# Performance work log

Measured on AMD Instinct MI355X. Metric: run time of the kernel, lower is better.

The kernel has to match this reference:

```python
import jax, jax.numpy as jnp
import numpy as np

N_HEAD = 16
HEAD_DIM = 64

def setup_inputs() -> dict:
    key = jax.random.key(0)
    k1, k2, k3 = jax.random.split(key, 3)
    B, S, D = 4, 2048, 1024
    x = jax.random.normal(k1, (B, S, D), dtype=jnp.float32)
    mask = jnp.tril(jnp.ones((S, S), dtype=bool))[None, None]  # (1,1,S,S) causal
    w_attn = jax.random.normal(k2, (D, 3 * D), dtype=jnp.float32) * (1.0 / np.sqrt(D))
    b_attn = jnp.zeros((3 * D,), dtype=jnp.float32)
    w_proj = jax.random.normal(k3, (D, D), dtype=jnp.float32) * (1.0 / np.sqrt(D))
    b_proj = jnp.zeros((D,), dtype=jnp.float32)
    return {"x": x, "mask": mask, "w_attn": w_attn, "b_attn": b_attn,
            "w_proj": w_proj, "b_proj": b_proj}

def reference(x, mask, w_attn, b_attn, w_proj, b_proj):
    B, S, D = x.shape
    H, hd = N_HEAD, HEAD_DIM
    qkv = x @ w_attn + b_attn                      # (B,S,3D)
    q, k, v = jnp.split(qkv, 3, axis=-1)
    q = q.reshape(B, S, H, hd).transpose(0, 2, 1, 3)  # (B,H,S,hd)
    k = k.reshape(B, S, H, hd).transpose(0, 2, 1, 3)
    v = v.reshape(B, S, H, hd).transpose(0, 2, 1, 3)
    scores = jnp.einsum('bhqd,bhkd->bhqk', q, k) / jnp.sqrt(jnp.float32(hd))
    scores = jnp.where(mask, scores, jnp.float32(-1e10))
    weights = jax.nn.softmax(scores, axis=-1)      # dropout is identity (deterministic=True)
    attn = jnp.einsum('bhqk,bhkd->bhqd', weights, v)
    attn = attn.transpose(0, 2, 1, 3).reshape(B, S, D)
    return attn @ w_proj + b_proj
```

## Files before the change

kernel.cpp:

```cpp
#include <hip/hip_runtime.h>
#include <hip/hip_bf16.h>
#include <stdint.h>


typedef uint16_t u16;
typedef __bf16 bf16x8 __attribute__((ext_vector_type(8)));
typedef __bf16 bf16x4 __attribute__((ext_vector_type(4)));
typedef short s16x4 __attribute__((ext_vector_type(4)));
typedef float f32x4 __attribute__((ext_vector_type(4)));

#define S_LEN 2048
#define DMODEL 1024
#define NHEAD 16
#define HDIM 64
#define MTOT 8192
#define NQKV 3072

__device__ __forceinline__ u16 f2bf(float f) {
    union { float f; uint32_t u; } v; v.f = f;
    uint32_t u = v.u;
    return (u16)((u + 0x7fffu + ((u >> 16) & 1u)) >> 16);
}

__device__ __forceinline__ s16x4 bits4(bf16x4 v) {
    union { bf16x4 b; s16x4 s; } u; u.b = v; return u.s;
}

__device__ __forceinline__ f32x4 mfma16(bf16x4 a, bf16x4 b, f32x4 c) {
    return __builtin_amdgcn_mfma_f32_16x16x16bf16_1k(bits4(a), bits4(b), c, 0, 0, 0);
}

__device__ __forceinline__ void async_load16(const void* g, void* l) {
    __builtin_amdgcn_global_load_lds(
        (__attribute__((address_space(1))) void*)g,
        (__attribute__((address_space(3))) void*)l,
        16, 0, 0);
}

__global__ void convert_x_kernel(const float4* __restrict__ in, ushort4* __restrict__ out, int n4) {
    int i = blockIdx.x * 256 + threadIdx.x;
    if (i < n4) {
        float4 f = in[i];
        ushort4 o;
        o.x = f2bf(f.x); o.y = f2bf(f.y); o.z = f2bf(f.z); o.w = f2bf(f.w);
        out[i] = o;
    }
}

__global__ void transpose_bf16_kernel(const float* __restrict__ in, u16* __restrict__ out, int R, int C) {
    __shared__ float tile[64][65];
    int r0 = blockIdx.y * 64, c0 = blockIdx.x * 64;
    #pragma unroll
    for (int i = 0; i < 16; ++i) {
        int idx = threadIdx.x + i * 256;
        int r = idx >> 6, c = idx & 63;
        tile[r][c] = in[(size_t)(r0 + r) * C + c0 + c];
    }
    __syncthreads();
    #pragma unroll
    for (int i = 0; i < 16; ++i) {
        int idx = threadIdx.x + i * 256;
        int c = idx >> 6, r = idx & 63;
        out[(size_t)(c0 + c) * R + r0 + r] = f2bf(tile[r][c]);
    }
}

__global__ void transpose_v_kernel(const u16* __restrict__ qkv, u16* __restrict__ vt) {
    __shared__ u16 tile[64 * 66];
    const int tid = threadIdx.x;
    const int stile = blockIdx.x, bh = blockIdx.y;
    const int b = bh >> 4, h = bh & 15;
    const u16* src = qkv + ((size_t)b * S_LEN + stile * 64) * NQKV + 2 * DMODEL + h * HDIM;
    #pragma unroll
    for (int it = 0; it < 2; ++it) {
        int item = it * 256 + tid;
        int s = item >> 3, d0 = (item & 7) * 8;
        bf16x8 v = *(const bf16x8*)(src + (size_t)s * NQKV + d0);
        const u16* vu = (const u16*)&v;
        #pragma unroll
        for (int j = 0; j < 8; ++j) tile[(d0 + j) * 66 + s] = vu[j];
    }
    __syncthreads();
    #pragma unroll
    for (int it = 0; it < 2; ++it) {
        int item = it * 256 + tid;
        int d = item >> 3, s0 = (item & 7) * 8;
        union { u16 u[8]; uint4 v; } pk;
        #pragma unroll
        for (int j = 0; j < 8; ++j) pk.u[j] = tile[d * 66 + s0 + j];
        *(uint4*)(vt + ((size_t)bh * 64 + d) * S_LEN + stile * 64 + s0) = pk.v;
    }
}

template<bool OUT_BF16>
__global__ __launch_bounds__(512, 2) void gemm256sq(
    const u16* __restrict__ A, const u16* __restrict__ Bt,
    const float* __restrict__ bias, void* __restrict__ C,
    int M, int N, int K)
{
    __shared__ __attribute__((aligned(16))) u16 sm[65536];
    u16* const As = sm;
    u16* const Bs = sm + 32768;

    const int tid = threadIdx.x;
    const int wave = tid >> 6, lane = tid & 63;
    const int l15 = lane & 15, q4 = lane >> 4;
    const int wm = wave >> 2, wn = wave & 3;

    const int bid = (int)blockIdx.x;
    const int xcd = bid & 7;
    const int lx  = bid >> 3;
    const int MB  = M >> 8;
    const int PM  = MB >> 3;
    const int nb  = lx / PM;
    const int mb  = xcd * PM + (lx - nb * PM);
    const int m0 = mb << 8, n0 = nb << 8;

    const u16* Ag = A + (size_t)m0 * K;
    const u16* Bg = Bt + (size_t)n0 * K;

    const int srow = tid >> 3;
    const size_t goff0 = (size_t)srow * K + (size_t)(((tid & 7) ^ (srow & 7)) * 8);
    const size_t goff1 = goff0 + (size_t)64 * K;
    const int ldso = tid * 8;

    const int ck0 = (q4 ^ (l15 & 7)) * 8;
    const int ck1 = ((4 + q4) ^ (l15 & 7)) * 8;
    const int rb0 = (wn * 64 + l15) * 64;

    f32x4 acc[8][4] = {};
    const int T = K >> 6;

#define STAGE_A(t_, h_) do { \
    const u16* g_ = Ag + (size_t)(h_) * 128 * K + (size_t)(t_) * 64; \
    u16* d_ = As + (((t_) & 1) * 2 + (h_)) * 8192; \
    async_load16(g_ + goff0, d_ + ldso); \
    async_load16(g_ + goff1, d_ + ldso + 4096); \
} while (0)

#define STAGE_B(t_, h_) do { \
    const u16* g_ = Bg + (size_t)(h_) * 128 * K + (size_t)(t_) * 64; \
    u16* d_ = Bs + ((t_) & 1) * 16384 + (h_) * 8192; \
    async_load16(g_ + goff0, d_ + ldso); \
    async_load16(g_ + goff1, d_ + ldso + 4096); \
} while (0)

#define LOAD_AF(P_) do { \
    af[0][0] = *(const bf16x8*)(Ah + ((2 * (P_)) * 16 + l15) * 64 + ck0); \
    af[0][1] = *(const bf16x8*)(Ah + ((2 * (P_)) * 16 + l15) * 64 + ck1); \
    af[1][0] = *(const bf16x8*)(Ah + ((2 * (P_) + 1) * 16 + l15) * 64 + ck0); \
    af[1][1] = *(const bf16x8*)(Ah + ((2 * (P_) + 1) * 16 + l15) * 64 + ck1); \
} while (0)

#define PHASE_MFMA(P_) do { \
    asm volatile("s_barrier" ::: "memory"); \
    __builtin_amdgcn_s_setprio(1); \
    _Pragma("unroll") \
    for (int i_ = 0; i_ < 2; ++i_) \
        _Pragma("unroll") \
        for (int nf_ = 0; nf_ < 4; ++nf_) \
            _Pragma("unroll") \
            for (int kk_ = 0; kk_ < 2; ++kk_) \
                acc[2 * (P_) + i_][nf_] = __builtin_amdgcn_mfma_f32_16x16x32_bf16( \
                    af[i_][kk_], bfr[nf_][kk_], acc[2 * (P_) + i_][nf_], 0, 0, 0); \
    __builtin_amdgcn_s_setprio(0); \
} while (0)

    STAGE_A(0, 0); STAGE_A(0, 1); STAGE_B(0, 0); STAGE_B(0, 1);
    if (T > 1) {
        STAGE_B(1, 0); STAGE_B(1, 1);
        asm volatile("s_waitcnt vmcnt(4)" ::: "memory");
    } else {
        asm volatile("s_waitcnt vmcnt(0)" ::: "memory");
    }
    asm volatile("s_barrier" ::: "memory");

    for (int t = 0; t < T; ++t) {
        const int par = t & 1;
        const u16* Ah = As + (par * 2 + wm) * 8192;
        const u16* Bl = Bs + par * 16384;

        bf16x8 af[2][2], bfr[4][2];

        #pragma unroll
        for (int nf = 0; nf < 4; ++nf) {
            bfr[nf][0] = *(const bf16x8*)(Bl + rb0 + nf * (16 * 64) + ck0);
            bfr[nf][1] = *(const bf16x8*)(Bl + rb0 + nf * (16 * 64) + ck1);
        }
        LOAD_AF(0);
        if (t + 1 < T) STAGE_A(t + 1, 0);
        PHASE_MFMA(0);
        asm volatile("s_barrier" ::: "memory");

        LOAD_AF(1);
        if (t + 1 < T) STAGE_A(t + 1, 1);
        PHASE_MFMA(1);
        asm volatile("s_barrier" ::: "memory");

        LOAD_AF(2);
        if (t + 2 < T) STAGE_B(t + 2, 0);
        PHASE_MFMA(2);
        asm volatile("s_barrier" ::: "memory");

        LOAD_AF(3);
        if (t + 2 < T) STAGE_B(t + 2, 1);
        PHASE_MFMA(3);
        if (t + 1 < T) {
            if (t + 2 < T) asm volatile("s_waitcnt vmcnt(4)" ::: "memory");
            else           asm volatile("s_waitcnt vmcnt(0)" ::: "memory");
            asm volatile("s_barrier" ::: "memory");
        }
    }

#undef STAGE_A
#undef STAGE_B
#undef LOAD_AF
#undef PHASE_MFMA

    #pragma unroll
    for (int mf = 0; mf < 8; ++mf) {
        const int row = m0 + wm * 128 + mf * 16 + q4 * 4;
        #pragma unroll
        for (int nf = 0; nf < 4; ++nf) {
            const int col = n0 + wn * 64 + nf * 16 + l15;
            const float bv = bias[col];
            #pragma unroll
            for (int r = 0; r < 4; ++r) {
                float v = acc[mf][nf][r] + bv;
                if (OUT_BF16) ((u16*)C)[(size_t)(row + r) * N + col] = f2bf(v);
                else          ((float*)C)[(size_t)(row + r) * N + col] = v;
            }
        }
    }
}

__device__ __forceinline__ void stage_tiles(
    const u16* __restrict__ qkv, const u16* __restrict__ vt,
    size_t base, int bh, int h, int w, int srow8, int schunk,
    int kt, u16* __restrict__ KsB, u16* __restrict__ VsB)
{
    #pragma unroll
    for (int q = 0; q < 2; ++q) {
        int rloc = w * 16 + q * 8 + srow8;
        int sc = ((schunk ^ (rloc & 7)) * 8);
        async_load16(qkv + (base + (size_t)kt * 64 + rloc) * (size_t)NQKV + DMODEL + h * HDIM + sc,
                     KsB + (w * 16 + q * 8) * 64);
        async_load16(vt + ((size_t)bh * 64 + rloc) * S_LEN + kt * 64 + sc,
                     VsB + (w * 16 + q * 8) * 64);
    }
}

__device__ __forceinline__ void attn_pass(
    int qt, const u16* __restrict__ qkv, const u16* __restrict__ vt,
    __bf16* __restrict__ outb, u16 (*Ks)[64 * 64], u16 (*Vs)[64 * 64],
    int w, int lane, int bh, int h, size_t base)
{
    const int l15 = lane & 15, q4 = lane >> 4;
    const int srow8 = lane >> 3, schunk = lane & 7;

    const float QSCALE = 0.125f * 1.44269504f;
    bf16x8 qf[2][2];
    #pragma unroll
    for (int mh = 0; mh < 2; ++mh) {
        int qrow = qt * 128 + mh * 64 + w * 16 + l15;
        #pragma unroll
        for (int kc = 0; kc < 2; ++kc) {
            bf16x8 raw = *(const bf16x8*)(qkv + (base + qrow) * (size_t)NQKV + h * HDIM + kc * 32 + q4 * 8);
            bf16x8 sc;
            #pragma unroll
            for (int j = 0; j < 8; ++j) sc[j] = (__bf16)((float)raw[j] * QSCALE);
            qf[mh][kc] = sc;
        }
    }

    bf16x4 ones4;
    #pragma unroll
    for (int j = 0; j < 4; ++j) ones4[j] = (__bf16)1.0f;

    f32x4 o0[4] = {}, o1[4] = {};
    f32x4 la0 = {}, la1 = {};

    const int ktlast = 2 * qt + 1;

    __syncthreads();
    stage_tiles(qkv, vt, base, bh, h, w, srow8, schunk, 0, Ks[0], Vs[0]);
    if (ktlast >= 1)
        stage_tiles(qkv, vt, base, bh, h, w, srow8, schunk, 1, Ks[1], Vs[1]);

    for (int kt = 0; kt <= 2 * qt; ++kt) {
        const int buf = kt % 3;
        __syncthreads();
        int pf = kt + 2;
        if (pf <= ktlast)
            stage_tiles(qkv, vt, base, bh, h, w, srow8, schunk, pf, Ks[pf % 3], Vs[pf % 3]);

        f32x4 st0[4] = {}, st1[4] = {};
        #pragma unroll
        for (int nt = 0; nt < 4; ++nt) {
            int n = nt * 16 + l15;
            #pragma unroll
            for (int kc = 0; kc < 2; ++kc) {
                int ch = (((kc * 4 + q4) ^ (n & 7)) * 8);
                bf16x8 kf = *(const bf16x8*)(&Ks[buf][n * 64 + ch]);
                st0[nt] = __builtin_amdgcn_mfma_f32_16x16x32_bf16(kf, qf[0][kc], st0[nt], 0, 0, 0);
                st1[nt] = __builtin_amdgcn_mfma_f32_16x16x32_bf16(kf, qf[1][kc], st1[nt], 0, 0, 0);
            }
        }

        if (kt == 2 * qt) {
            #pragma unroll
            for (int nt = 0; nt < 4; ++nt)
                #pragma unroll
                for (int r = 0; r < 4; ++r) {
                    int keyl = nt * 16 + q4 * 4 + r;
                    if (keyl > w * 16 + l15) st0[nt][r] = -1e30f;
                }
        }

        bf16x4 pb0[4], pb1[4];
        #pragma unroll
        for (int nt = 0; nt < 4; ++nt)
            #pragma unroll
            for (int r = 0; r < 4; ++r) {
                pb0[nt][r] = (__bf16)__builtin_amdgcn_exp2f(st0[nt][r]);
                pb1[nt][r] = (__bf16)__builtin_amdgcn_exp2f(st1[nt][r]);
            }

        #pragma unroll
        for (int nt = 0; nt < 4; ++nt) {
            #pragma unroll
            for (int mt = 0; mt < 4; ++mt) {
                int row = mt * 16 + l15;
                int ch = (nt * 2 + (q4 >> 1)) ^ (row & 7);
                bf16x4 vf = *(const bf16x4*)(&Vs[buf][row * 64 + ch * 8 + (q4 & 1) * 4]);
                o0[mt] = mfma16(vf, pb0[nt], o0[mt]);
                o1[mt] = mfma16(vf, pb1[nt], o1[mt]);
            }
            la0 = mfma16(ones4, pb0[nt], la0);
            la1 = mfma16(ones4, pb1[nt], la1);
        }
    }

    {
        const int buf = ktlast % 3;
        __syncthreads();

        f32x4 st1[4] = {};
        #pragma unroll
        for (int nt = 0; nt < 4; ++nt) {
            int n = nt * 16 + l15;
            #pragma unroll
            for (int kc = 0; kc < 2; ++kc) {
                int ch = (((kc * 4 + q4) ^ (n & 7)) * 8);
                bf16x8 kf = *(const bf16x8*)(&Ks[buf][n * 64 + ch]);
                st1[nt] = __builtin_amdgcn_mfma_f32_16x16x32_bf16(kf, qf[1][kc], st1[nt], 0, 0, 0);
            }
        }
        bf16x4 pb1[4];
        #pragma unroll
        for (int nt = 0; nt < 4; ++nt)
            #pragma unroll
            for (int r = 0; r < 4; ++r) {
                int keyl = nt * 16 + q4 * 4 + r;
                float s = (keyl > w * 16 + l15) ? -1e30f : st1[nt][r];
                pb1[nt][r] = (__bf16)__builtin_amdgcn_exp2f(s);
            }
        #pragma unroll
        for (int nt = 0; nt < 4; ++nt) {
            #pragma unroll
            for (int mt = 0; mt < 4; ++mt) {
                int row = mt * 16 + l15;
                int ch = (nt * 2 + (q4 >> 1)) ^ (row & 7);
                bf16x4 vf = *(const bf16x4*)(&Vs[buf][row * 64 + ch * 8 + (q4 & 1) * 4]);
                o1[mt] = mfma16(vf, pb1[nt], o1[mt]);
            }
            la1 = mfma16(ones4, pb1[nt], la1);
        }
    }

    float inv0 = 1.0f / la0[0], inv1 = 1.0f / la1[0];
    int row0 = qt * 128 + w * 16 + l15;
    int row1 = row0 + 64;
    #pragma unroll
    for (int mt = 0; mt < 4; ++mt) {
        union { __bf16 b[4]; ushort4 v; } p0, p1;
        #pragma unroll
        for (int r = 0; r < 4; ++r) {
            p0.b[r] = (__bf16)(o0[mt][r] * inv0);
            p1.b[r] = (__bf16)(o1[mt][r] * inv1);
        }
        int col = h * HDIM + mt * 16 + q4 * 4;
        *(ushort4*)(&outb[(base + row0) * (size_t)DMODEL + col]) = p0.v;
        *(ushort4*)(&outb[(base + row1) * (size_t)DMODEL + col]) = p1.v;
    }
}

__global__ __launch_bounds__(256, 3) void attn_kernel(
    const u16* __restrict__ qkv, const u16* __restrict__ vt, u16* __restrict__ out)
{
    __shared__ __attribute__((aligned(16))) u16 Ks[3][64 * 64];
    __shared__ __attribute__((aligned(16))) u16 Vs[3][64 * 64];

    const int tid = threadIdx.x;
    const int w = tid >> 6, lane = tid & 63;
    const int bh = blockIdx.y;
    const int b = bh >> 4, h = bh & 15;
    const size_t base = (size_t)b * S_LEN;
    const int NT = (int)gridDim.x * 2;

    attn_pass(NT - 1 - (int)blockIdx.x, qkv, vt, (__bf16*)out, Ks, Vs, w, lane, bh, h, base);
    attn_pass((int)blockIdx.x,          qkv, vt, (__bf16*)out, Ks, Vs, w, lane, bh, h, base);
}

extern "C" void kernel_launch(void* const* d_in, const int* in_sizes, int n_in,
                              void* d_out, int out_size, void* d_ws, size_t ws_size,
                              hipStream_t stream) {
    const float* x      = (const float*)d_in[0];
    const float* w_attn = (const float*)d_in[2];
    const float* b_attn = (const float*)d_in[3];
    const float* w_proj = (const float*)d_in[4];
    const float* b_proj = (const float*)d_in[5];

    u16* xb   = (u16*)d_ws;
    u16* wat  = xb  + (size_t)MTOT * DMODEL;
    u16* wpt  = wat + (size_t)NQKV * DMODEL;
    u16* qkv  = wpt + (size_t)DMODEL * DMODEL;
    u16* attn = qkv + (size_t)MTOT * NQKV;
    u16* vt   = xb;

    convert_x_kernel<<<(MTOT * DMODEL / 4 + 255) / 256, 256, 0, stream>>>(
        (const float4*)x, (ushort4*)xb, MTOT * DMODEL / 4);
    transpose_bf16_kernel<<<dim3(NQKV / 64, DMODEL / 64), 256, 0, stream>>>(w_attn, wat, DMODEL, NQKV);
    transpose_bf16_kernel<<<dim3(DMODEL / 64, DMODEL / 64), 256, 0, stream>>>(w_proj, wpt, DMODEL, DMODEL);

    gemm256sq<true><<<dim3((MTOT / 256) * (NQKV / 256)), 512, 0, stream>>>(
        xb, wat, b_attn, (void*)qkv, MTOT, NQKV, DMODEL);

    transpose_v_kernel<<<dim3(S_LEN / 64, 4 * NHEAD), 256, 0, stream>>>(qkv, vt);

    attn_kernel<<<dim3(S_LEN / 256, 4 * NHEAD), 256, 0, stream>>>(qkv, vt, attn);

    gemm256sq<false><<<dim3((MTOT / 256) * (DMODEL / 256)), 512, 0, stream>>>(
        attn, wpt, b_proj, d_out, MTOT, DMODEL, DMODEL);
}
```

Measured before the change: 278.7 us.

## Switch GEMMs to 32x32x16 MFMA and use 256x128 tiles for projection

Rewrites the tiled GEMM to use 32x32x16 bf16 MFMA instructions with per-wave 32-row subtiles, changing the fragment loads and epilogue layout. The kernel is templated on the number of M subtiles, so the output projection can use 256x128 tiles. That doubles its block count (32x8=256 blocks) to fill the CUs better. Larger MFMAs reduce LDS fragment traffic per FLOP, at the cost of a new epilogue mapping and an extra lgkmcnt wait.

```diff
diff --git a/kernel.cpp b/kernel.cpp
--- a/kernel.cpp
+++ b/kernel.cpp
@@ -8,6 +8,7 @@
 typedef __bf16 bf16x4 __attribute__((ext_vector_type(4)));
 typedef short s16x4 __attribute__((ext_vector_type(4)));
 typedef float f32x4 __attribute__((ext_vector_type(4)));
+typedef float f32x16 __attribute__((ext_vector_type(16)));
 
 #define S_LEN 2048
 #define DMODEL 1024
@@ -28,6 +29,10 @@
 
 __device__ __forceinline__ f32x4 mfma16(bf16x4 a, bf16x4 b, f32x4 c) {
     return __builtin_amdgcn_mfma_f32_16x16x16bf16_1k(bits4(a), bits4(b), c, 0, 0, 0);
+}
+
+__device__ __forceinline__ f32x16 mfma32(bf16x8 a, bf16x8 b, f32x16 c) {
+    return __builtin_amdgcn_mfma_f32_32x32x16_bf16(a, b, c, 0, 0, 0);
 }
 
 __device__ __forceinline__ void async_load16(const void* g, void* l) {
@@ -92,20 +97,23 @@
     }
 }
 
-template<bool OUT_BF16>
-__global__ __launch_bounds__(512, 2) void gemm256sq(
+template<int MSUB, bool OUT_BF16>
+__global__ __launch_bounds__(512, 2) void gemm32(
     const u16* __restrict__ A, const u16* __restrict__ Bt,
     const float* __restrict__ bias, void* __restrict__ C,
     int M, int N, int K)
 {
-    __shared__ __attribute__((aligned(16))) u16 sm[65536];
+    constexpr int NBH = MSUB / 2;
+    constexpr int BSLOT = 64 * MSUB * 64;
+    __shared__ __attribute__((aligned(16))) u16 sm[32768 + 2 * BSLOT];
     u16* const As = sm;
     u16* const Bs = sm + 32768;
 
     const int tid = threadIdx.x;
     const int wave = tid >> 6, lane = tid & 63;
-    const int l15 = lane & 15, q4 = lane >> 4;
-    const int wm = wave >> 2, wn = wave & 3;
+    const int l31 = lane & 31, hi = lane >> 5;
+    const int wm = wave / MSUB, wn = wave % MSUB;
+    const int wmbase = wm * MSUB * 32;
 
     const int bid = (int)blockIdx.x;
     const int xcd = bid & 7;
@@ -114,7 +122,7 @@
     const int PM  = MB >> 3;
     const int nb  = lx / PM;
     const int mb  = xcd * PM + (lx - nb * PM);
-    const int m0 = mb << 8, n0 = nb << 8;
+    const int m0 = mb << 8, n0 = nb * 64 * MSUB;
 
     const u16* Ag = A + (size_t)m0 * K;
     const u16* Bg = Bt + (size_t)n0 * K;
@@ -124,52 +132,52 @@
     const size_t goff1 = goff0 + (size_t)64 * K;
     const int ldso = tid * 8;
 
-    const int ck0 = (q4 ^ (l15 & 7)) * 8;
-    const int ck1 = ((4 + q4) ^ (l15 & 7)) * 8;
-    const int rb0 = (wn * 64 + l15) * 64;
-
-    f32x4 acc[8][4] = {};
+    const int ck[4] = { ((0 + hi) ^ (lane & 7)) * 8, ((2 + hi) ^ (lane & 7)) * 8,
+                        ((4 + hi) ^ (lane & 7)) * 8, ((6 + hi) ^ (lane & 7)) * 8 };
+    const int AH = wmbase >> 7;
+    const int abase = (wmbase & 127) + l31;
+    const int bbase = wn * 64 + l31;
+
+    f32x16 acc[MSUB][2] = {};
     const int T = K >> 6;
 
 #define STAGE_A(t_, h_) do { \
-    const u16* g_ = Ag + (size_t)(h_) * 128 * K + (size_t)(t_) * 64; \
-    u16* d_ = As + (((t_) & 1) * 2 + (h_)) * 8192; \
-    async_load16(g_ + goff0, d_ + ldso); \
-    async_load16(g_ + goff1, d_ + ldso + 4096); \
+    const u16* ga_ = Ag + (size_t)(h_) * 128 * K + (size_t)(t_) * 64; \
+    u16* da_ = As + (((t_) & 1) * 2 + (h_)) * 8192; \
+    async_load16(ga_ + goff0, da_ + ldso); \
+    async_load16(ga_ + goff1, da_ + ldso + 4096); \
 } while (0)
 
 #define STAGE_B(t_, h_) do { \
-    const u16* g_ = Bg + (size_t)(h_) * 128 * K + (size_t)(t_) * 64; \
-    u16* d_ = Bs + ((t_) & 1) * 16384 + (h_) * 8192; \
-    async_load16(g_ + goff0, d_ + ldso); \
-    async_load16(g_ + goff1, d_ + ldso + 4096); \
+    const u16* gb_ = Bg + (size_t)(h_) * 128 * K + (size_t)(t_) * 64; \
+    u16* db_ = Bs + ((t_) & 1) * BSLOT + (h_) * 8192; \
+    async_load16(gb_ + goff0, db_ + ldso); \
+    async_load16(gb_ + goff1, db_ + ldso + 4096); \
 } while (0)
 
-#define LOAD_AF(P_) do { \
-    af[0][0] = *(const bf16x8*)(Ah + ((2 * (P_)) * 16 + l15) * 64 + ck0); \
-    af[0][1] = *(const bf16x8*)(Ah + ((2 * (P_)) * 16 + l15) * 64 + ck1); \
-    af[1][0] = *(const bf16x8*)(Ah + ((2 * (P_) + 1) * 16 + l15) * 64 + ck0); \
-    af[1][1] = *(const bf16x8*)(Ah + ((2 * (P_) + 1) * 16 + l15) * 64 + ck1); \
+#define LOAD_AF(S_) do { \
+    _Pragma("unroll") \
+    for (int i_ = 0; i_ < MSUB; ++i_) \
+        af[i_] = *(const bf16x8*)(Ah + (abase + i_ * 32) * 64 + ck[S_]); \
 } while (0)
 
-#define PHASE_MFMA(P_) do { \
+#define PHASE_MFMA(S_) do { \
     asm volatile("s_barrier" ::: "memory"); \
     __builtin_amdgcn_s_setprio(1); \
     _Pragma("unroll") \
-    for (int i_ = 0; i_ < 2; ++i_) \
+    for (int i_ = 0; i_ < MSUB; ++i_) \
         _Pragma("unroll") \
-        for (int nf_ = 0; nf_ < 4; ++nf_) \
-            _Pragma("unroll") \
-            for (int kk_ = 0; kk_ < 2; ++kk_) \
-                acc[2 * (P_) + i_][nf_] = __builtin_amdgcn_mfma_f32_16x16x32_bf16( \
-                    af[i_][kk_], bfr[nf_][kk_], acc[2 * (P_) + i_][nf_], 0, 0, 0); \
+        for (int n_ = 0; n_ < 2; ++n_) \
+            acc[i_][n_] = mfma32(af[i_], bfr[n_][S_], acc[i_][n_]); \
     __builtin_amdgcn_s_setprio(0); \
 } while (0)
 
-    STAGE_A(0, 0); STAGE_A(0, 1); STAGE_B(0, 0); STAGE_B(0, 1);
+    STAGE_A(0, 0); STAGE_A(0, 1);
+    STAGE_B(0, 0); if constexpr (NBH == 2) STAGE_B(0, 1);
     if (T > 1) {
-        STAGE_B(1, 0); STAGE_B(1, 1);
-        asm volatile("s_waitcnt vmcnt(4)" ::: "memory");
+        STAGE_B(1, 0); if constexpr (NBH == 2) STAGE_B(1, 1);
+        if constexpr (NBH == 2) asm volatile("s_waitcnt vmcnt(4)" ::: "memory");
+        else                    asm volatile("s_waitcnt vmcnt(2)" ::: "memory");
     } else {
         asm volatile("s_waitcnt vmcnt(0)" ::: "memory");
     }
@@ -177,24 +185,30 @@
 
     for (int t = 0; t < T; ++t) {
         const int par = t & 1;
-        const u16* Ah = As + (par * 2 + wm) * 8192;
-        const u16* Bl = Bs + par * 16384;
-
-        bf16x8 af[2][2], bfr[4][2];
-
-        #pragma unroll
-        for (int nf = 0; nf < 4; ++nf) {
-            bfr[nf][0] = *(const bf16x8*)(Bl + rb0 + nf * (16 * 64) + ck0);
-            bfr[nf][1] = *(const bf16x8*)(Bl + rb0 + nf * (16 * 64) + ck1);
+        const u16* Ah = As + (par * 2 + AH) * 8192;
+        const u16* Bl = Bs + par * BSLOT;
+
+        bf16x8 af[MSUB], bfr[2][4];
+
+        #pragma unroll
+        for (int n_ = 0; n_ < 2; ++n_) {
+            bfr[n_][0] = *(const bf16x8*)(Bl + (bbase + n_ * 32) * 64 + ck[0]);
+            bfr[n_][1] = *(const bf16x8*)(Bl + (bbase + n_ * 32) * 64 + ck[1]);
         }
         LOAD_AF(0);
         if (t + 1 < T) STAGE_A(t + 1, 0);
         PHASE_MFMA(0);
         asm volatile("s_barrier" ::: "memory");
 
+        #pragma unroll
+        for (int n_ = 0; n_ < 2; ++n_) {
+            bfr[n_][2] = *(const bf16x8*)(Bl + (bbase + n_ * 32) * 64 + ck[2]);
+            bfr[n_][3] = *(const bf16x8*)(Bl + (bbase + n_ * 32) * 64 + ck[3]);
+        }
         LOAD_AF(1);
         if (t + 1 < T) STAGE_A(t + 1, 1);
         PHASE_MFMA(1);
+        asm volatile("s_waitcnt lgkmcnt(0)" ::: "memory");
         asm volatile("s_barrier" ::: "memory");
 
         LOAD_AF(2);
@@ -203,11 +217,15 @@
         asm volatile("s_barrier" ::: "memory");
 
         LOAD_AF(3);
-        if (t + 2 < T) STAGE_B(t + 2, 1);
+        if constexpr (NBH == 2) { if (t + 2 < T) STAGE_B(t + 2, 1); }
         PHASE_MFMA(3);
         if (t + 1 < T) {
-            if (t + 2 < T) asm volatile("s_waitcnt vmcnt(4)" ::: "memory");
-            else           asm volatile("s_waitcnt vmcnt(0)" ::: "memory");
+            if (t + 2 < T) {
+                if constexpr (NBH == 2) asm volatile("s_waitcnt vmcnt(4)" ::: "memory");
+                else                    asm volatile("s_waitcnt vmcnt(2)" ::: "memory");
+            } else {
+                asm volatile("s_waitcnt vmcnt(0)" ::: "memory");
+            }
             asm volatile("s_barrier" ::: "memory");
         }
     }
@@ -218,17 +236,20 @@
 #undef PHASE_MFMA
 
     #pragma unroll
-    for (int mf = 0; mf < 8; ++mf) {
-        const int row = m0 + wm * 128 + mf * 16 + q4 * 4;
-        #pragma unroll
-        for (int nf = 0; nf < 4; ++nf) {
-            const int col = n0 + wn * 64 + nf * 16 + l15;
+    for (int i = 0; i < MSUB; ++i) {
+        #pragma unroll
+        for (int n = 0; n < 2; ++n) {
+            const int col = n0 + wn * 64 + n * 32 + l31;
             const float bv = bias[col];
             #pragma unroll
-            for (int r = 0; r < 4; ++r) {
-                float v = acc[mf][nf][r] + bv;
-                if (OUT_BF16) ((u16*)C)[(size_t)(row + r) * N + col] = f2bf(v);
-                else          ((float*)C)[(size_t)(row + r) * N + col] = v;
+            for (int g = 0; g < 4; ++g) {
+                #pragma unroll
+                for (int r = 0; r < 4; ++r) {
+                    const int row = m0 + wmbase + i * 32 + g * 8 + r + 4 * hi;
+                    float v = acc[i][n][g * 4 + r] + bv;
+                    if (OUT_BF16) ((u16*)C)[(size_t)row * N + col] = f2bf(v);
+                    else          ((float*)C)[(size_t)row * N + col] = v;
+                }
             }
         }
     }
@@ -433,13 +454,13 @@
     transpose_bf16_kernel<<<dim3(NQKV / 64, DMODEL / 64), 256, 0, stream>>>(w_attn, wat, DMODEL, NQKV);
     transpose_bf16_kernel<<<dim3(DMODEL / 64, DMODEL / 64), 256, 0, stream>>>(w_proj, wpt, DMODEL, DMODEL);
 
-    gemm256sq<true><<<dim3((MTOT / 256) * (NQKV / 256)), 512, 0, stream>>>(
+    gemm32<4, true><<<dim3((MTOT / 256) * (NQKV / 256)), 512, 0, stream>>>(
         xb, wat, b_attn, (void*)qkv, MTOT, NQKV, DMODEL);
 
     transpose_v_kernel<<<dim3(S_LEN / 64, 4 * NHEAD), 256, 0, stream>>>(qkv, vt);
 
     attn_kernel<<<dim3(S_LEN / 256, 4 * NHEAD), 256, 0, stream>>>(qkv, vt, attn);
 
-    gemm256sq<false><<<dim3((MTOT / 256) * (DMODEL / 256)), 512, 0, stream>>>(
+    gemm32<2, false><<<dim3((MTOT / 256) * (DMODEL / 128)), 512, 0, stream>>>(
         attn, wpt, b_proj, d_out, MTOT, DMODEL, DMODEL);
 }
```

Measured after the change: 273.7 us. Within noise of the previous version (-1.8%).
